# Optimization experiments

Measured on AMD Instinct MI355X. Metric: run time of the kernel, lower is better.

The kernel has to match this reference:

```python
import jax, jax.numpy as jnp
import numpy as np

DN = ('NCHW', 'OIHW', 'NCHW')


def conv2d(x, w, b):
    y = jax.lax.conv_general_dilated(x, w, (1, 1), 'SAME', dimension_numbers=DN)
    return y + b[None, :, None, None]


def dyn_filter(x, Wa, ba, Wb, bb, Wc, bc):
    # KPN-style head: predict 81 per-pixel 9x9 filter taps, softmax-normalized.
    h = jax.nn.relu(conv2d(x, Wa, ba))
    h = jax.nn.relu(conv2d(h, Wb, bb))
    f = conv2d(h, Wc, bc)            # (N, 81, H, W)
    return jax.nn.softmax(f, axis=1)


def apply_dynamic_conv(x, f):
    # Equivalent to pad(4) + unfold(9x9) + mul + sum, without materializing
    # the (N,81,H,W)*... patch tensor: accumulate 81 shifted slices.
    N, C, H, W = x.shape  # C == 1
    xp = jnp.pad(x, ((0, 0), (0, 0), (4, 4), (4, 4)))
    out = jnp.zeros((N, 1, H, W), x.dtype)
    for dy in range(9):
        for dx in range(9):
            k = dy * 9 + dx  # matches unfold(2).unfold(3).permute(0,1,4,5,2,3) tap order
            out = out + xp[:, :, dy:dy + H, dx:dx + W] * f[:, k:k + 1]
    return out


def nearest_resize(x, oh, ow):
    _, _, ih, iw = x.shape
    ri = jnp.arange(oh) * ih // oh   # matches torch F.interpolate mode='nearest'
    rj = jnp.arange(ow) * iw // ow
    return x[:, :, ri][:, :, :, rj]


def setup_inputs() -> dict:
    key = jax.random.key(0)
    ks = jax.random.split(key, 8)
    s = 0.05
    return {
        'x': jax.random.normal(ks[0], (2, 1, 512, 512), jnp.float32),
        'g': jax.random.normal(ks[1], (2, 1, 512, 512), jnp.float32),
        'fWa': jax.random.normal(ks[2], (5, 64, 1, 3, 3), jnp.float32) * s,
        'fba': jnp.zeros((5, 64), jnp.float32),
        'fWb': jax.random.normal(ks[3], (5, 64, 64, 3, 3), jnp.float32) * s,
        'fbb': jnp.zeros((5, 64), jnp.float32),
        'fWc': jax.random.normal(ks[4], (5, 81, 64, 3, 3), jnp.float32) * s,
        'fbc': jnp.zeros((5, 81), jnp.float32),
        'W2a': jax.random.normal(ks[5], (64, 5, 3, 3), jnp.float32) * s,
        'b2a': jnp.zeros((64,), jnp.float32),
        'W2b': jax.random.normal(ks[6], (1, 64, 3, 3), jnp.float32) * s,
        'b2b': jnp.zeros((1,), jnp.float32),
    }


def reference(x, g, fWa, fba, fWb, fbb, fWc, fbc, W2a, b2a, W2b, b2b):
    N, C, h, w = x.shape
    scales = [
        x,
        nearest_resize(x, h // 2, w // 2),
        nearest_resize(x, h // 4, w // 4),
        nearest_resize(x, h // 8, w // 8),
        g,
    ]
    outs = []
    for i, s in enumerate(scales):
        f = dyn_filter(s, fWa[i], fba[i], fWb[i], fbb[i], fWc[i], fbc[i])
        y = apply_dynamic_conv(s, f)
        if y.shape[2] != h or y.shape[3] != w:
            y = nearest_resize(y, h, w)
        outs.append(y)
    cat = jnp.concatenate(outs, axis=1)  # (N, 5, h, w)
    hid = jax.nn.relu(conv2d(cat, W2a, b2a))
    return conv2d(hid, W2b, b2b)
```

## Files before the change

### kernel.cpp

```cpp
#include <hip/hip_runtime.h>
#include <math.h>

typedef _Float16 half8 __attribute__((ext_vector_type(8)));
typedef _Float16 half4v __attribute__((ext_vector_type(4)));
typedef float f32x4 __attribute__((ext_vector_type(4)));

#define LOG2E 1.44269504f

__device__ __forceinline__ void pack_generic(int rem, int NT, int COUT, float scale,
                                             const float* __restrict__ src,
                                             _Float16* __restrict__ dst) {
  int j = rem & 7, lane = (rem >> 3) & 63, rest = rem >> 9;
  int t = rest % NT, s = rest / NT;
  int oc = t * 16 + (lane & 15);
  int tap = s >> 1;
  int ic = (s & 1) * 32 + ((lane >> 4) & 3) * 8 + j;
  float v = (oc < COUT) ? src[((size_t)oc * 64 + ic) * 9 + tap] * scale : 0.f;
  dst[rem] = (_Float16)v;
}

__global__ void prep_all_kernel(const float* __restrict__ fWa, const float* __restrict__ fWb,
                                const float* __restrict__ fWc, const float* __restrict__ W2a,
                                const float* __restrict__ W2b, const float* __restrict__ x,
                                _Float16* __restrict__ Bp1, _Float16* __restrict__ BpA,
                                _Float16* __restrict__ BpB, _Float16* __restrict__ Bpb,
                                _Float16* __restrict__ Bpc,
                                _Float16* __restrict__ s1, _Float16* __restrict__ s2,
                                _Float16* __restrict__ s3) {
  int idx = blockIdx.x * blockDim.x + threadIdx.x;
  if (idx < 184320) {
    int sc = idx / 36864, rem = idx - sc * 36864;
    pack_generic(rem, 4, 64, 1.f, fWb + sc * 36864, Bpb + sc * 36864);
  } else if (idx < 460800) {
    int i2 = idx - 184320;
    int sc = i2 / 55296, rem = i2 - sc * 55296;
    pack_generic(rem, 6, 81, LOG2E, fWc + sc * 46656, Bpc + sc * 55296);
  } else if (idx < 471040) {
    int i2 = idx - 460800;
    int sc = i2 >> 11, rem = i2 & 2047;
    int j = rem & 7, lane = (rem >> 3) & 63, nt = rem >> 9;
    int oc = nt * 16 + (lane & 15);
    int k = ((lane >> 4) & 3) * 8 + j;
    float v = (k < 9) ? fWa[sc * 576 + oc * 9 + k] : 0.f;
    Bp1[sc * 2048 + rem] = (_Float16)v;
  } else if (idx < 475136) {
    int rem = idx - 471040;
    int j = rem & 7, lane = (rem >> 3) & 63;
    int nt = (rem >> 9) & 3, s = rem >> 11;
    int oc = nt * 16 + (lane & 15);
    int k = s * 32 + ((lane >> 4) & 3) * 8 + j;
    float v = 0.f;
    if (k < 45) { int ic = k / 9, tap = k - ic * 9; v = W2a[(oc * 5 + ic) * 9 + tap]; }
    BpA[rem] = (_Float16)v;
  } else if (idx < 484352) {
    pack_generic(idx - 475136, 1, 1, 1.f, W2b, BpB);
  } else if (idx < 615424) {
    int i2 = idx - 484352;
    int n = i2 >> 16, p = i2 & 65535, rr = p >> 8, cc = p & 255;
    s1[i2] = (_Float16)x[(size_t)n * 262144 + (size_t)(rr * 2) * 512 + cc * 2];
  } else if (idx < 648192) {
    int i2 = idx - 615424;
    int n = i2 >> 14, p = i2 & 16383, rr = p >> 7, cc = p & 127;
    s2[i2] = (_Float16)x[(size_t)n * 262144 + (size_t)(rr * 4) * 512 + cc * 4];
  } else if (idx < 656384) {
    int i2 = idx - 648192;
    int n = i2 >> 12, p = i2 & 4095, rr = p >> 6, cc = p & 63;
    s3[i2] = (_Float16)x[(size_t)n * 262144 + (size_t)(rr * 8) * 512 + cc * 8];
  }
}

__device__ __forceinline__ int xcd_swizzle(int bid) {
  return (bid & 7) * 596 + (bid >> 3);
}

__device__ __forceinline__ void map_block(int bid, int& sc, int& n, int& bx, int& by,
                                          int& Hs, int& RS, int& h2off) {
  if (bid < 2048) { sc = 0; Hs = 512; RS = 1; h2off = 0;
    int t = bid; n = t >> 10; t &= 1023; by = t >> 5; bx = t & 31; }
  else if (bid < 4096) { sc = 4; Hs = 512; RS = 1; h2off = 33554432;
    int t = bid - 2048; n = t >> 10; t &= 1023; by = t >> 5; bx = t & 31; }
  else if (bid < 4608) { sc = 1; Hs = 256; RS = 2; h2off = 67108864;
    int t = bid - 4096; n = t >> 8; t &= 255; by = t >> 4; bx = t & 15; }
  else if (bid < 4736) { sc = 2; Hs = 128; RS = 4; h2off = 75497472;
    int t = bid - 4608; n = t >> 6; t &= 63; by = t >> 3; bx = t & 7; }
  else { sc = 3; Hs = 64; RS = 8; h2off = 77594624;
    int t = bid - 4736; n = t >> 4; t &= 15; by = t >> 2; bx = t & 3; }
}

__device__ __forceinline__ const void* pick_src(int sc, const float* x, const float* g,
                                                const _Float16* s1, const _Float16* s2,
                                                const _Float16* s3, int& sStr, bool& f16s) {
  if (sc == 0) { sStr = 262144; f16s = false; return x; }
  if (sc == 1) { sStr = 65536; f16s = true; return s1; }
  if (sc == 2) { sStr = 16384; f16s = true; return s2; }
  if (sc == 3) { sStr = 4096; f16s = true; return s3; }
  sStr = 262144; f16s = false; return g;
}

__device__ __forceinline__ float src_load(const void* p, bool f16s, size_t off) {
  return f16s ? (float)((const _Float16*)p)[off] : ((const float*)p)[off];
}

template <int NT, bool SWAP>
__device__ __forceinline__ void mfma_acc18(const _Float16* slab, const half8* __restrict__ Bp,
                                           f32x4 (&acc)[4][NT], int tid) {
  const int lane = tid & 63;
  const int wv = tid >> 6;
  const int quad = lane >> 4;
  const int ln15 = lane & 15;
  const f32x4 zz = {0.f, 0.f, 0.f, 0.f};
#pragma unroll
  for (int mt = 0; mt < 4; ++mt)
#pragma unroll
    for (int nt = 0; nt < NT; ++nt) acc[mt][nt] = zz;
  auto step = [&](int s, half8 (&bf)[NT]) {
    const int tap = s >> 1;
    const int dy = tap / 3;
    const int dx = tap - dy * 3;
    const int C = dx + ln15;
    const int qsw = (((s & 1) * 4 + quad) ^ (C & 7));
    const _Float16* base = slab + C * 64 + qsw * 8;
    half8 af[4];
#pragma unroll
    for (int mt = 0; mt < 4; ++mt)
      af[mt] = *(const half8*)(base + (wv * 4 + mt + dy) * (18 * 64));
#pragma unroll
    for (int mt = 0; mt < 4; ++mt)
#pragma unroll
      for (int nt = 0; nt < NT; ++nt)
        acc[mt][nt] = SWAP
          ? __builtin_amdgcn_mfma_f32_16x16x32_f16(bf[nt], af[mt], acc[mt][nt], 0, 0, 0)
          : __builtin_amdgcn_mfma_f32_16x16x32_f16(af[mt], bf[nt], acc[mt][nt], 0, 0, 0);
  };
  half8 bA[NT], bB[NT];
#pragma unroll
  for (int nt = 0; nt < NT; ++nt) bA[nt] = Bp[nt * 64 + lane];
#pragma unroll 1
  for (int i = 0; i < 9; ++i) {
    const int s0 = 2 * i, s1 = 2 * i + 1;
    const int s2 = (s1 + 1 < 18) ? s1 + 1 : 17;
#pragma unroll
    for (int nt = 0; nt < NT; ++nt) bB[nt] = Bp[(s1 * NT + nt) * 64 + lane];
    step(s0, bA);
#pragma unroll
    for (int nt = 0; nt < NT; ++nt) bA[nt] = Bp[(s2 * NT + nt) * 64 + lane];
    step(s1, bB);
  }
}

template <int NT, int COUT, int COUTP, bool RELU, typename OutT>
__device__ __forceinline__ void mfma_body(const _Float16* slab, const half8* __restrict__ Bp,
                                          const float* __restrict__ bias,
                                          OutT* __restrict__ out,
                                          int H, int W, int gr0, int gc0, int tid) {
  f32x4 acc[4][NT];
  mfma_acc18<NT, false>(slab, Bp, acc, tid);
  const int lane = tid & 63;
  const int wv = tid >> 6;
  const int quad = lane >> 4;
  const int ln15 = lane & 15;
  float bvv[NT];
#pragma unroll
  for (int nt = 0; nt < NT; ++nt) {
    const int oc = nt * 16 + ln15;
    bvv[nt] = (oc < COUT) ? bias[oc] : 0.f;
  }
#pragma unroll
  for (int mt = 0; mt < 4; ++mt) {
    const int gr = gr0 + wv * 4 + mt;
#pragma unroll
    for (int reg = 0; reg < 4; ++reg) {
      const int gc = gc0 + quad * 4 + reg;
#pragma unroll
      for (int nt = 0; nt < NT; ++nt) {
        const int oc = nt * 16 + ln15;
        float v = acc[mt][nt][reg] + bvv[nt];
        if (RELU) v = fmaxf(v, 0.f);
        if (oc < COUTP) out[((size_t)gr * W + gc) * COUTP + oc] = (OutT)v;
      }
    }
  }
}

__global__ __launch_bounds__(256)
void conv12_ms_kernel(const float* __restrict__ x, const float* __restrict__ g,
                      const _Float16* __restrict__ s1, const _Float16* __restrict__ s2,
                      const _Float16* __restrict__ s3,
                      const half8* __restrict__ Bp1b, const float* __restrict__ fba,
                      const half8* __restrict__ Bpbb, const float* __restrict__ fbb,
                      _Float16* __restrict__ h2) {
  __shared__ float xs[20 * 20];
  __shared__ __align__(16) _Float16 slab[18 * 18 * 64];
  int sc, n, bx, by, Hs, RS, h2off;
  map_block(xcd_swizzle(blockIdx.x), sc, n, bx, by, Hs, RS, h2off);
  int sStr; bool f16s;
  const void* src = pick_src(sc, x, g, s1, s2, s3, sStr, f16s);
  _Float16* out = h2 + h2off + (size_t)n * Hs * Hs * 64;
  const half8* Bp1 = Bp1b + sc * 256;
  const half8* Bp = Bpbb + sc * 4608;
  const float* ba = fba + sc * 64;
  const float* bb = fbb + sc * 64;
  const int H = Hs, W = Hs;
  const int tid = threadIdx.x;
  const int gr0 = by * 16, gc0 = bx * 16;
  for (int i = tid; i < 400; i += 256) {
    int R = i / 20, C = i % 20;
    int gr = gr0 - 2 + R, gc = gc0 - 2 + C;
    xs[i] = (gr >= 0 && gr < H && gc >= 0 && gc < W)
                ? src_load(src, f16s, (size_t)n * sStr + (size_t)gr * W + gc) : 0.f;
  }
  __syncthreads();
  const int lane = tid & 63;
  const int wv = tid >> 6;
  const int quad = lane >> 4;
  const int ln15 = lane & 15;
  half8 bf1[4];
  float b1v[4][4];
#pragma unroll
  for (int nt = 0; nt < 4; ++nt) {
    bf1[nt] = Bp1[nt * 64 + lane];
#pragma unroll
    for (int reg = 0; reg < 4; ++reg) b1v[nt][reg] = ba[nt * 16 + quad * 4 + reg];
  }
  int off1[8];
  bool v1[8];
#pragma unroll
  for (int j = 0; j < 8; ++j) {
    int k = quad * 8 + j;
    v1[j] = (k < 9);
    off1[j] = v1[j] ? ((k / 3) * 20 + (k % 3)) : 0;
  }
  const f32x4 zz = {0.f, 0.f, 0.f, 0.f};
#pragma unroll 1
  for (int mt = wv; mt < 21; mt += 4) {
    int p = mt * 16 + ln15;
    int pcl = (p < 323) ? p : 323;
    int Rg = pcl / 18, Cg = pcl - Rg * 18;
    int base = Rg * 20 + Cg;
    half8 af;
#pragma unroll
    for (int j = 0; j < 8; ++j)
      af[j] = v1[j] ? (_Float16)xs[base + off1[j]] : (_Float16)0.f;
    f32x4 a1[4] = {zz, zz, zz, zz};
#pragma unroll
    for (int nt = 0; nt < 4; ++nt)
      a1[nt] = __builtin_amdgcn_mfma_f32_16x16x32_f16(bf1[nt], af, a1[nt], 0, 0, 0);
    if (p < 324) {
      int R2 = p / 18, C2 = p - R2 * 18;
      int gr = gr0 - 1 + R2, gc = gc0 - 1 + C2;
      bool inb = (gr >= 0 && gr < H && gc >= 0 && gc < W);
      _Float16* sb = slab + p * 64 + (quad & 1) * 4;
      const int csw = C2 & 7;
#pragma unroll
      for (int nt = 0; nt < 4; ++nt) {
        half4v w;
#pragma unroll
        for (int reg = 0; reg < 4; ++reg) {
          float v = inb ? fmaxf(a1[nt][reg] + b1v[nt][reg], 0.f) : 0.f;
          w[reg] = (_Float16)v;
        }
        const int chunk = nt * 2 + (quad >> 1);
        *(half4v*)(sb + ((chunk ^ csw) * 8)) = w;
      }
    }
  }
  __syncthreads();
  mfma_body<4, 64, 64, true, _Float16>(slab, Bp, bb, out, H, W, gr0, gc0, tid);
}

__global__ __launch_bounds__(256)
void conv3sd_ms_kernel(const _Float16* __restrict__ h2, const half8* __restrict__ Bpcb,
                       const float* __restrict__ fbc,
                       const float* __restrict__ x, const float* __restrict__ g,
                       const _Float16* __restrict__ s1, const _Float16* __restrict__ s2,
                       const _Float16* __restrict__ s3, float* __restrict__ cat) {
  __shared__ __align__(16) _Float16 slab[324 * 40];
  __shared__ float xs[24 * 24];
  int sc, n, bx, by, Hs, RS, h2off;
  map_block(xcd_swizzle(blockIdx.x), sc, n, bx, by, Hs, RS, h2off);
  int sStr; bool f16s;
  const void* src = pick_src(sc, x, g, s1, s2, s3, sStr, f16s);
  const _Float16* in = h2 + h2off + (size_t)n * Hs * Hs * 64;
  const half8* Bp = Bpcb + sc * 6912;
  const float* bias = fbc + sc * 81;
  float* catp = cat + (size_t)(sc * 2 + n) * 262144;
  const int H = Hs, W = Hs;
  const int tid = threadIdx.x;
  const int gr0 = by * 16, gc0 = bx * 16;
  const int lane = tid & 63;
  const int wv = tid >> 6;
  const int quad = lane >> 4;
  const int ln15 = lane & 15;
  for (int i = tid; i < 576; i += 256) {
    int R = i / 24, C = i % 24;
    int gr = gr0 - 4 + R, gc = gc0 - 4 + C;
    xs[i] = (gr >= 0 && gr < H && gc >= 0 && gc < W)
                ? src_load(src, f16s, (size_t)n * sStr + (size_t)gr * W + gc) : 0.f;
  }
  f32x4 acc[4][6];
  const f32x4 zz = {0.f, 0.f, 0.f, 0.f};
#pragma unroll
  for (int mt = 0; mt < 4; ++mt)
#pragma unroll
    for (int nt = 0; nt < 6; ++nt) acc[mt][nt] = zz;
#pragma unroll 1
  for (int h = 0; h < 2; ++h) {
    if (h) __syncthreads();
    for (int i = tid; i < 1296; i += 256) {
      int chunk = i & 3, px = i >> 2;
      int R = px / 18, C = px - R * 18;
      int gr = gr0 - 1 + R, gc = gc0 - 1 + C;
      half8 v = {0, 0, 0, 0, 0, 0, 0, 0};
      if (gr >= 0 && gr < H && gc >= 0 && gc < W)
        v = *(const half8*)(in + ((size_t)gr * W + gc) * 64 + (h * 4 + chunk) * 8);
      *(half8*)(slab + px * 40 + chunk * 8) = v;
    }
    __syncthreads();
    auto ctap = [&](int tap, half8 (&bf)[6]) {
      const int dy = tap / 3;
      const int dx = tap - dy * 3;
      const int C = dx + ln15;
      const _Float16* base = slab + C * 40 + quad * 8;
      half8 af[4];
#pragma unroll
      for (int mt = 0; mt < 4; ++mt)
        af[mt] = *(const half8*)(base + (wv * 4 + mt + dy) * 720);
#pragma unroll
      for (int mt = 0; mt < 4; ++mt)
#pragma unroll
        for (int nt = 0; nt < 6; ++nt)
          acc[mt][nt] = __builtin_amdgcn_mfma_f32_16x16x32_f16(bf[nt], af[mt], acc[mt][nt], 0, 0, 0);
    };
    half8 bA[6], bB[6];
#pragma unroll
    for (int nt = 0; nt < 6; ++nt) bA[nt] = Bp[(h * 6 + nt) * 64 + lane];
#pragma unroll 1
    for (int i = 0; i < 4; ++i) {
      const int t1 = 2 * i + 1, t2 = 2 * i + 2;
#pragma unroll
      for (int nt = 0; nt < 6; ++nt) bB[nt] = Bp[(((t1 * 2 + h) * 6) + nt) * 64 + lane];
      ctap(2 * i, bA);
#pragma unroll
      for (int nt = 0; nt < 6; ++nt) bA[nt] = Bp[(((t2 * 2 + h) * 6) + nt) * 64 + lane];
      ctap(t1, bB);
    }
    ctap(8, bA);
  }
  float bvv[6][4];
  int dyx[6][4];
  bool vv[6][4];
#pragma unroll
  for (int nt = 0; nt < 6; ++nt)
#pragma unroll
    for (int reg = 0; reg < 4; ++reg) {
      int ch = nt * 16 + quad * 4 + reg;
      bool ok = (ch < 81);
      vv[nt][reg] = ok;
      bvv[nt][reg] = ok ? bias[ch] * LOG2E : 0.f;
      int dy = ch / 9, dx = ch - dy * 9;
      dyx[nt][reg] = ok ? dy * 24 + dx : 0;
    }
  const int lrs = (RS == 2) ? 1 : ((RS == 4) ? 2 : 3);
#pragma unroll
  for (int mt = 0; mt < 4; ++mt) {
    const float* xb = xs + (wv * 4 + mt) * 24 + ln15;
    float sum = 0.f, y = 0.f;
#pragma unroll
    for (int nt = 0; nt < 6; ++nt)
#pragma unroll
      for (int reg = 0; reg < 4; ++reg) {
        if (vv[nt][reg]) {
          float e = exp2f(acc[mt][nt][reg] + bvv[nt][reg]);
          sum += e;
          y = fmaf(e, xb[dyx[nt][reg]], y);
        }
      }
    sum += __shfl_xor(sum, 16, 64);
    sum += __shfl_xor(sum, 32, 64);
    y += __shfl_xor(y, 16, 64);
    y += __shfl_xor(y, 32, 64);
    const float o = y / sum;
    const int gr = gr0 + wv * 4 + mt, gc = gc0 + ln15;
    if (RS == 1) {
      if (quad == 0) catp[(size_t)gr * 512 + gc] = o;
    } else {
      for (int t = quad; t < RS * RS; t += 4) {
        int a = t >> lrs, b = t & (RS - 1);
        catp[((size_t)(gr * RS + a)) * 512 + (gc * RS + b)] = o;
      }
    }
  }
}

__global__ __launch_bounds__(256)
void tail_fused_kernel(const float* __restrict__ cat,
                       const half8* __restrict__ BpA, const float* __restrict__ b2a,
                       const half8* __restrict__ BpB, const float* __restrict__ b2b,
                       float* __restrict__ out) {
  __shared__ float cs[20 * 20 * 5];
  __shared__ __align__(16) _Float16 hid[18 * 18 * 64];
  const int n = blockIdx.z;
  float* op = out + (size_t)n * (512 * 512);
  const int tid = threadIdx.x;
  const int gr0 = blockIdx.y * 16, gc0 = blockIdx.x * 16;
  for (int i = tid; i < 2000; i += 256) {
    int ic = i / 400, px = i - ic * 400;
    int R = px / 20, C = px - R * 20;
    int gr = gr0 - 2 + R, gc = gc0 - 2 + C;
    cs[px * 5 + ic] = (gr >= 0 && gr < 512 && gc >= 0 && gc < 512)
                ? cat[(size_t)(ic * 2 + n) * 262144 + (size_t)gr * 512 + gc] : 0.f;
  }
  __syncthreads();
  const int lane = tid & 63;
  const int wv = tid >> 6;
  const int quad = lane >> 4;
  const int ln15 = lane & 15;
  int goff[2][8];
  bool gok[2][8];
#pragma unroll
  for (int s = 0; s < 2; ++s)
#pragma unroll
    for (int j = 0; j < 8; ++j) {
      int k = s * 32 + quad * 8 + j;
      bool ok = (k < 45);
      int ic = k / 9;
      int tap = k - ic * 9;
      int dy = tap / 3, dx = tap - dy * 3;
      goff[s][j] = ok ? ((dy * 20 + dx) * 5 + ic) : 0;
      gok[s][j] = ok;
    }
  half8 bfA[2][4];
  float bAv[4][4];
#pragma unroll
  for (int s = 0; s < 2; ++s)
#pragma unroll
    for (int nt = 0; nt < 4; ++nt) bfA[s][nt] = BpA[(s * 4 + nt) * 64 + lane];
#pragma unroll
  for (int nt = 0; nt < 4; ++nt)
#pragma unroll
    for (int reg = 0; reg < 4; ++reg) bAv[nt][reg] = b2a[nt * 16 + quad * 4 + reg];
  const f32x4 zz = {0.f, 0.f, 0.f, 0.f};
#pragma unroll 1
  for (int mt = wv; mt < 21; mt += 4) {
    int p = mt * 16 + ln15;
    int pcl = (p < 323) ? p : 323;
    int base = (pcl / 18) * 100 + (pcl % 18) * 5;
    f32x4 acc1[4] = {zz, zz, zz, zz};
#pragma unroll
    for (int s = 0; s < 2; ++s) {
      half8 af;
#pragma unroll
      for (int j = 0; j < 8; ++j) {
        float a = gok[s][j] ? cs[base + goff[s][j]] : 0.f;
        af[j] = (_Float16)a;
      }
#pragma unroll
      for (int nt = 0; nt < 4; ++nt)
        acc1[nt] = __builtin_amdgcn_mfma_f32_16x16x32_f16(bfA[s][nt], af, acc1[nt], 0, 0, 0);
    }
    if (p < 324) {
      int R2 = p / 18, C2 = p - R2 * 18;
      int gr = gr0 - 1 + R2, gc = gc0 - 1 + C2;
      bool inb = (gr >= 0 && gr < 512 && gc >= 0 && gc < 512);
      _Float16* sb = hid + p * 64 + (quad & 1) * 4;
      const int csw = C2 & 7;
#pragma unroll
      for (int nt = 0; nt < 4; ++nt) {
        half4v w;
#pragma unroll
        for (int reg = 0; reg < 4; ++reg) {
          float v = inb ? fmaxf(acc1[nt][reg] + bAv[nt][reg], 0.f) : 0.f;
          w[reg] = (_Float16)v;
        }
        const int chunk = nt * 2 + (quad >> 1);
        *(half4v*)(sb + ((chunk ^ csw) * 8)) = w;
      }
    }
  }
  __syncthreads();
  mfma_body<1, 1, 1, false, float>(hid, BpB, b2b, op, 512, 512, gr0, gc0, tid);
}

extern "C" void kernel_launch(void* const* d_in, const int* in_sizes, int n_in,
                              void* d_out, int out_size, void* d_ws, size_t ws_size,
                              hipStream_t stream) {
  (void)in_sizes; (void)n_in; (void)out_size; (void)ws_size;
  const float* x   = (const float*)d_in[0];
  const float* g   = (const float*)d_in[1];
  const float* fWa = (const float*)d_in[2];
  const float* fba = (const float*)d_in[3];
  const float* fWb = (const float*)d_in[4];
  const float* fbb = (const float*)d_in[5];
  const float* fWc = (const float*)d_in[6];
  const float* fbc = (const float*)d_in[7];
  const float* W2a = (const float*)d_in[8];
  const float* b2a = (const float*)d_in[9];
  const float* W2b = (const float*)d_in[10];
  const float* b2b = (const float*)d_in[11];
  float* out = (float*)d_out;
  float* ws = (float*)d_ws;

  float* Bp1F = ws;
  float* BpAF = Bp1F + 5120;
  float* BpBF = BpAF + 2048;
  float* BpbF = BpBF + 4608;
  float* BpcF = BpbF + 92160;
  float* s1F  = BpcF + 138240;
  float* s2F  = s1F + 65536;
  float* s3F  = s2F + 16384;
  float* cat  = s3F + 4096;
  float* h2F  = cat + 2621440;
  _Float16* s1 = (_Float16*)s1F;
  _Float16* s2 = (_Float16*)s2F;
  _Float16* s3 = (_Float16*)s3F;
  _Float16* h2 = (_Float16*)h2F;
  const half8* Bp1 = (const half8*)Bp1F;
  const half8* BpA = (const half8*)BpAF;
  const half8* BpB = (const half8*)BpBF;
  const half8* Bpb = (const half8*)BpbF;
  const half8* Bpc = (const half8*)BpcF;

  prep_all_kernel<<<2564, 256, 0, stream>>>(fWa, fWb, fWc, W2a, W2b, x,
                                            (_Float16*)Bp1F, (_Float16*)BpAF,
                                            (_Float16*)BpBF, (_Float16*)BpbF,
                                            (_Float16*)BpcF, s1, s2, s3);
  conv12_ms_kernel<<<4768, 256, 0, stream>>>(x, g, s1, s2, s3, Bp1, fba, Bpb, fbb, h2);
  conv3sd_ms_kernel<<<4768, 256, 0, stream>>>(h2, Bpc, fbc, x, g, s1, s2, s3, cat);
  tail_fused_kernel<<<dim3(32, 32, 2), 256, 0, stream>>>(cat, BpA, b2a, BpB, b2b, out);
}
```

Before: 390.5 us.

## Double block size to 512 threads and prefetch second channel half in conv3

All three main kernels now launch 512-thread blocks (8 waves), and each wave handles 2 row-tiles instead of 4. This halves per-wave accumulator registers and raises the number of waves per tile. In conv3sd, the second channel-half slab is loaded into registers before the first half's taps run, then written to shared memory afterwards, so the global load overlaps MFMA work. The cost is more waves contending for LDS, an extra barrier, and lower per-wave reuse of B fragments across row tiles.

```diff
diff --git a/kernel.cpp b/kernel.cpp
--- a/kernel.cpp
+++ b/kernel.cpp
@@ -101,16 +101,16 @@
   return f16s ? (float)((const _Float16*)p)[off] : ((const float*)p)[off];
 }
 
-template <int NT, bool SWAP>
+template <int MT, int NT, bool SWAP>
 __device__ __forceinline__ void mfma_acc18(const _Float16* slab, const half8* __restrict__ Bp,
-                                           f32x4 (&acc)[4][NT], int tid) {
+                                           f32x4 (&acc)[MT][NT], int tid) {
   const int lane = tid & 63;
   const int wv = tid >> 6;
   const int quad = lane >> 4;
   const int ln15 = lane & 15;
   const f32x4 zz = {0.f, 0.f, 0.f, 0.f};
 #pragma unroll
-  for (int mt = 0; mt < 4; ++mt)
+  for (int mt = 0; mt < MT; ++mt)
 #pragma unroll
     for (int nt = 0; nt < NT; ++nt) acc[mt][nt] = zz;
   auto step = [&](int s, half8 (&bf)[NT]) {
@@ -120,12 +120,12 @@
     const int C = dx + ln15;
     const int qsw = (((s & 1) * 4 + quad) ^ (C & 7));
     const _Float16* base = slab + C * 64 + qsw * 8;
-    half8 af[4];
-#pragma unroll
-    for (int mt = 0; mt < 4; ++mt)
-      af[mt] = *(const half8*)(base + (wv * 4 + mt + dy) * (18 * 64));
-#pragma unroll
-    for (int mt = 0; mt < 4; ++mt)
+    half8 af[MT];
+#pragma unroll
+    for (int mt = 0; mt < MT; ++mt)
+      af[mt] = *(const half8*)(base + (wv * MT + mt + dy) * (18 * 64));
+#pragma unroll
+    for (int mt = 0; mt < MT; ++mt)
 #pragma unroll
       for (int nt = 0; nt < NT; ++nt)
         acc[mt][nt] = SWAP
@@ -148,13 +148,13 @@
   }
 }
 
-template <int NT, int COUT, int COUTP, bool RELU, typename OutT>
+template <int MT, int NT, int COUT, int COUTP, bool RELU, typename OutT>
 __device__ __forceinline__ void mfma_body(const _Float16* slab, const half8* __restrict__ Bp,
                                           const float* __restrict__ bias,
                                           OutT* __restrict__ out,
                                           int H, int W, int gr0, int gc0, int tid) {
-  f32x4 acc[4][NT];
-  mfma_acc18<NT, false>(slab, Bp, acc, tid);
+  f32x4 acc[MT][NT];
+  mfma_acc18<MT, NT, false>(slab, Bp, acc, tid);
   const int lane = tid & 63;
   const int wv = tid >> 6;
   const int quad = lane >> 4;
@@ -166,8 +166,8 @@
     bvv[nt] = (oc < COUT) ? bias[oc] : 0.f;
   }
 #pragma unroll
-  for (int mt = 0; mt < 4; ++mt) {
-    const int gr = gr0 + wv * 4 + mt;
+  for (int mt = 0; mt < MT; ++mt) {
+    const int gr = gr0 + wv * MT + mt;
 #pragma unroll
     for (int reg = 0; reg < 4; ++reg) {
       const int gc = gc0 + quad * 4 + reg;
@@ -182,7 +182,7 @@
   }
 }
 
-__global__ __launch_bounds__(256)
+__global__ __launch_bounds__(512, 4)
 void conv12_ms_kernel(const float* __restrict__ x, const float* __restrict__ g,
                       const _Float16* __restrict__ s1, const _Float16* __restrict__ s2,
                       const _Float16* __restrict__ s3,
@@ -203,7 +203,7 @@
   const int H = Hs, W = Hs;
   const int tid = threadIdx.x;
   const int gr0 = by * 16, gc0 = bx * 16;
-  for (int i = tid; i < 400; i += 256) {
+  for (int i = tid; i < 400; i += 512) {
     int R = i / 20, C = i % 20;
     int gr = gr0 - 2 + R, gc = gc0 - 2 + C;
     xs[i] = (gr >= 0 && gr < H && gc >= 0 && gc < W)
@@ -232,7 +232,7 @@
   }
   const f32x4 zz = {0.f, 0.f, 0.f, 0.f};
 #pragma unroll 1
-  for (int mt = wv; mt < 21; mt += 4) {
+  for (int mt = wv; mt < 21; mt += 8) {
     int p = mt * 16 + ln15;
     int pcl = (p < 323) ? p : 323;
     int Rg = pcl / 18, Cg = pcl - Rg * 18;
@@ -265,15 +265,16 @@
     }
   }
   __syncthreads();
-  mfma_body<4, 64, 64, true, _Float16>(slab, Bp, bb, out, H, W, gr0, gc0, tid);
-}
-
-__global__ __launch_bounds__(256)
+  mfma_body<2, 4, 64, 64, true, _Float16>(slab, Bp, bb, out, H, W, gr0, gc0, tid);
+}
+
+__global__ __launch_bounds__(512, 4)
 void conv3sd_ms_kernel(const _Float16* __restrict__ h2, const half8* __restrict__ Bpcb,
                        const float* __restrict__ fbc,
                        const float* __restrict__ x, const float* __restrict__ g,
                        const _Float16* __restrict__ s1, const _Float16* __restrict__ s2,
                        const _Float16* __restrict__ s3, float* __restrict__ cat) {
+  constexpr int MT = 2;
   __shared__ __align__(16) _Float16 slab[324 * 40];
   __shared__ float xs[24 * 24];
   int sc, n, bx, by, Hs, RS, h2off;
@@ -291,46 +292,57 @@
   const int wv = tid >> 6;
   const int quad = lane >> 4;
   const int ln15 = lane & 15;
-  for (int i = tid; i < 576; i += 256) {
+  for (int i = tid; i < 576; i += 512) {
     int R = i / 24, C = i % 24;
     int gr = gr0 - 4 + R, gc = gc0 - 4 + C;
     xs[i] = (gr >= 0 && gr < H && gc >= 0 && gc < W)
                 ? src_load(src, f16s, (size_t)n * sStr + (size_t)gr * W + gc) : 0.f;
   }
-  f32x4 acc[4][6];
-  const f32x4 zz = {0.f, 0.f, 0.f, 0.f};
-#pragma unroll
-  for (int mt = 0; mt < 4; ++mt)
-#pragma unroll
-    for (int nt = 0; nt < 6; ++nt) acc[mt][nt] = zz;
-#pragma unroll 1
-  for (int h = 0; h < 2; ++h) {
-    if (h) __syncthreads();
-    for (int i = tid; i < 1296; i += 256) {
+  auto stage_load = [&](int h, half8 (&stg)[3], int (&soff)[3], bool (&sok)[3]) {
+#pragma unroll
+    for (int it = 0; it < 3; ++it) {
+      int i = tid + it * 512;
+      bool ok = (i < 1296);
       int chunk = i & 3, px = i >> 2;
       int R = px / 18, C = px - R * 18;
       int gr = gr0 - 1 + R, gc = gc0 - 1 + C;
       half8 v = {0, 0, 0, 0, 0, 0, 0, 0};
-      if (gr >= 0 && gr < H && gc >= 0 && gc < W)
+      if (ok && gr >= 0 && gr < H && gc >= 0 && gc < W)
         v = *(const half8*)(in + ((size_t)gr * W + gc) * 64 + (h * 4 + chunk) * 8);
-      *(half8*)(slab + px * 40 + chunk * 8) = v;
-    }
-    __syncthreads();
-    auto ctap = [&](int tap, half8 (&bf)[6]) {
-      const int dy = tap / 3;
-      const int dx = tap - dy * 3;
-      const int C = dx + ln15;
-      const _Float16* base = slab + C * 40 + quad * 8;
-      half8 af[4];
-#pragma unroll
-      for (int mt = 0; mt < 4; ++mt)
-        af[mt] = *(const half8*)(base + (wv * 4 + mt + dy) * 720);
-#pragma unroll
-      for (int mt = 0; mt < 4; ++mt)
-#pragma unroll
-        for (int nt = 0; nt < 6; ++nt)
-          acc[mt][nt] = __builtin_amdgcn_mfma_f32_16x16x32_f16(bf[nt], af[mt], acc[mt][nt], 0, 0, 0);
-    };
+      stg[it] = v;
+      soff[it] = px * 40 + chunk * 8;
+      sok[it] = ok;
+    }
+  };
+  auto stage_write = [&](half8 (&stg)[3], int (&soff)[3], bool (&sok)[3]) {
+#pragma unroll
+    for (int it = 0; it < 3; ++it)
+      if (sok[it]) *(half8*)(slab + soff[it]) = stg[it];
+  };
+
+  f32x4 acc[MT][6];
+  const f32x4 zz = {0.f, 0.f, 0.f, 0.f};
+#pragma unroll
+  for (int mt = 0; mt < MT; ++mt)
+#pragma unroll
+    for (int nt = 0; nt < 6; ++nt) acc[mt][nt] = zz;
+
+  auto ctap = [&](int tap, half8 (&bf)[6]) {
+    const int dy = tap / 3;
+    const int dx = tap - dy * 3;
+    const int C = dx + ln15;
+    const _Float16* base = slab + C * 40 + quad * 8;
+    half8 af[MT];
+#pragma unroll
+    for (int mt = 0; mt < MT; ++mt)
+      af[mt] = *(const half8*)(base + (wv * MT + mt + dy) * 720);
+#pragma unroll
+    for (int mt = 0; mt < MT; ++mt)
+#pragma unroll
+      for (int nt = 0; nt < 6; ++nt)
+        acc[mt][nt] = __builtin_amdgcn_mfma_f32_16x16x32_f16(bf[nt], af[mt], acc[mt][nt], 0, 0, 0);
+  };
+  auto run_taps = [&](int h) {
     half8 bA[6], bB[6];
 #pragma unroll
     for (int nt = 0; nt < 6; ++nt) bA[nt] = Bp[(h * 6 + nt) * 64 + lane];
@@ -345,7 +357,20 @@
       ctap(t1, bB);
     }
     ctap(8, bA);
-  }
+  };
+
+  half8 stgA[3]; int soffA[3]; bool sokA[3];
+  half8 stgB[3]; int soffB[3]; bool sokB[3];
+  stage_load(0, stgA, soffA, sokA);
+  stage_write(stgA, soffA, sokA);
+  __syncthreads();
+  stage_load(1, stgB, soffB, sokB);
+  run_taps(0);
+  __syncthreads();
+  stage_write(stgB, soffB, sokB);
+  __syncthreads();
+  run_taps(1);
+
   float bvv[6][4];
   int dyx[6][4];
   bool vv[6][4];
@@ -362,8 +387,8 @@
     }
   const int lrs = (RS == 2) ? 1 : ((RS == 4) ? 2 : 3);
 #pragma unroll
-  for (int mt = 0; mt < 4; ++mt) {
-    const float* xb = xs + (wv * 4 + mt) * 24 + ln15;
+  for (int mt = 0; mt < MT; ++mt) {
+    const float* xb = xs + (wv * MT + mt) * 24 + ln15;
     float sum = 0.f, y = 0.f;
 #pragma unroll
     for (int nt = 0; nt < 6; ++nt)
@@ -380,7 +405,7 @@
     y += __shfl_xor(y, 16, 64);
     y += __shfl_xor(y, 32, 64);
     const float o = y / sum;
-    const int gr = gr0 + wv * 4 + mt, gc = gc0 + ln15;
+    const int gr = gr0 + wv * MT + mt, gc = gc0 + ln15;
     if (RS == 1) {
       if (quad == 0) catp[(size_t)gr * 512 + gc] = o;
     } else {
@@ -392,7 +417,7 @@
   }
 }
 
-__global__ __launch_bounds__(256)
+__global__ __launch_bounds__(512, 4)
 void tail_fused_kernel(const float* __restrict__ cat,
                        const half8* __restrict__ BpA, const float* __restrict__ b2a,
                        const half8* __restrict__ BpB, const float* __restrict__ b2b,
@@ -403,7 +428,7 @@
   float* op = out + (size_t)n * (512 * 512);
   const int tid = threadIdx.x;
   const int gr0 = blockIdx.y * 16, gc0 = blockIdx.x * 16;
-  for (int i = tid; i < 2000; i += 256) {
+  for (int i = tid; i < 2000; i += 512) {
     int ic = i / 400, px = i - ic * 400;
     int R = px / 20, C = px - R * 20;
     int gr = gr0 - 2 + R, gc = gc0 - 2 + C;
@@ -441,7 +466,7 @@
     for (int reg = 0; reg < 4; ++reg) bAv[nt][reg] = b2a[nt * 16 + quad * 4 + reg];
   const f32x4 zz = {0.f, 0.f, 0.f, 0.f};
 #pragma unroll 1
-  for (int mt = wv; mt < 21; mt += 4) {
+  for (int mt = wv; mt < 21; mt += 8) {
     int p = mt * 16 + ln15;
     int pcl = (p < 323) ? p : 323;
     int base = (pcl / 18) * 100 + (pcl % 18) * 5;
@@ -478,7 +503,7 @@
     }
   }
   __syncthreads();
-  mfma_body<1, 1, 1, false, float>(hid, BpB, b2b, op, 512, 512, gr0, gc0, tid);
+  mfma_body<2, 1, 1, 1, false, float>(hid, BpB, b2b, op, 512, 512, gr0, gc0, tid);
 }
 
 extern "C" void kernel_launch(void* const* d_in, const int* in_sizes, int n_in,
@@ -524,7 +549,7 @@
                                             (_Float16*)Bp1F, (_Float16*)BpAF,
                                             (_Float16*)BpBF, (_Float16*)BpbF,
                                             (_Float16*)BpcF, s1, s2, s3);
-  conv12_ms_kernel<<<4768, 256, 0, stream>>>(x, g, s1, s2, s3, Bp1, fba, Bpb, fbb, h2);
-  conv3sd_ms_kernel<<<4768, 256, 0, stream>>>(h2, Bpc, fbc, x, g, s1, s2, s3, cat);
-  tail_fused_kernel<<<dim3(32, 32, 2), 256, 0, stream>>>(cat, BpA, b2a, BpB, b2b, out);
-}
+  conv12_ms_kernel<<<4768, 512, 0, stream>>>(x, g, s1, s2, s3, Bp1, fba, Bpb, fbb, h2);
+  conv3sd_ms_kernel<<<4768, 512, 0, stream>>>(h2, Bpc, fbc, x, g, s1, s2, s3, cat);
+  tail_fused_kernel<<<dim3(32, 32, 2), 512, 0, stream>>>(cat, BpA, b2a, BpB, b2b, out);
+}
```

Result: no change. 393.0 us (+0.6%).
